# Kernel tuning notes

Measured on AMD Instinct MI355X. Metric: run time of the kernel, lower is better.

The kernel has to match this reference:

```python
import jax, jax.numpy as jnp
import numpy as np
from jax.scipy.ndimage import map_coordinates

# Geometry (parallel-beam analogue of the astra projector in the source)
NUMPIX = 256          # image is NUMPIX x NUMPIX
NUMBIN = 367          # detector bins (~ NUMPIX*sqrt(2), 1-pixel spacing)
NUMTHETA = 360        # projection angles over [0, 360) deg
NS = 4                # number of ordered subsets (angles j::NS per subset)
NT = 367              # samples along each ray (covers image diagonal)
BETA = 1.0            # relaxation parameter
DX = 1.0              # pixel size
THRESHOLD = 0.01      # IterativeLayer residual threshold
MAX_ITERS = 2         # IterativeLayer max_iterations
EPS = float(np.finfo(np.float64).eps)
DEN_EPS = 1e-6        # guard for Minv/Dinv denominators

_theta = np.deg2rad(np.arange(NUMTHETA) * (360.0 / NUMTHETA)).astype(np.float32)
_COS = jnp.asarray(np.cos(_theta), dtype=jnp.float32)
_SIN = jnp.asarray(np.sin(_theta), dtype=jnp.float32)
_CDET = (NUMBIN - 1) / 2.0
_CPIX = (NUMPIX - 1) / 2.0
_S = jnp.arange(NUMBIN, dtype=jnp.float32) - _CDET          # detector coords
_T = jnp.arange(NT, dtype=jnp.float32) - (NT - 1) / 2.0     # along-ray coords
_pix = jnp.arange(NUMPIX, dtype=jnp.float32) - _CPIX
_Y, _X = jnp.meshgrid(_pix, _pix, indexing='ij')            # pixel centers


def forward_project(f, ca, sa):
    # Radon transform of f for angles (ca, sa): line integral along each ray.
    # coords: [na, NUMBIN, NT]
    x = _S[None, :, None] * ca[:, None, None] - _T[None, None, :] * sa[:, None, None]
    y = _S[None, :, None] * sa[:, None, None] + _T[None, None, :] * ca[:, None, None]
    vals = map_coordinates(f, [y + _CPIX, x + _CPIX], order=1, mode='constant', cval=0.0)
    return vals.sum(-1)  # [na, NUMBIN]


def backproject(g, ca, sa):
    # Adjoint-style backprojection of sinogram g [na, NUMBIN] onto the image grid.
    def one(ga, c, s_):
        sd = _X * c + _Y * s_ + _CDET                      # [NUMPIX, NUMPIX]
        i0 = jnp.floor(sd)
        w = sd - i0
        i0i = i0.astype(jnp.int32)
        v0 = jnp.where((i0i >= 0) & (i0i < NUMBIN), ga[jnp.clip(i0i, 0, NUMBIN - 1)], 0.0)
        i1i = i0i + 1
        v1 = jnp.where((i1i >= 0) & (i1i < NUMBIN), ga[jnp.clip(i1i, 0, NUMBIN - 1)], 0.0)
        return v0 * (1.0 - w) + v1 * w
    return jax.vmap(one)(g, ca, sa).sum(0)


def sart_reconstruct(f, sino):
    # Precompute SART normalizers per subset: Minv = A_j(1_img), Dinv = A_j^T(1_sino).
    cas = [_COS[j::NS] for j in range(NS)]
    sas = [_SIN[j::NS] for j in range(NS)]
    ones_img = jnp.ones((NUMPIX, NUMPIX), dtype=f.dtype)
    Minv = [jnp.maximum(forward_project(ones_img, cas[j], sas[j]), DEN_EPS) for j in range(NS)]
    Dinv = [jnp.maximum(backproject(jnp.ones_like(sino[j::NS]), cas[j], sas[j]), DEN_EPS) for j in range(NS)]

    for _ in range(MAX_ITERS):
        # inner denoiser layer modeled as identity
        fk = f
        for j in range(NS):  # one SART ordered-subset sweep
            fp = forward_project(fk, cas[j], sas[j])
            diffs = (sino[j::NS] - fp * DX) / Minv[j] / DX
            bp = backproject(diffs, cas[j], sas[j])
            bp = jnp.where(jnp.abs(bp) > 1000.0, 0.0, bp)
            fk = fk + BETA * bp / Dinv[j]
        fk = jnp.maximum(fk, EPS)
        # residual ||A fk * dx - sino||_F, computed subset-by-subset
        res2 = jnp.float32(0.0)
        for j in range(NS):
            fpj = forward_project(fk, cas[j], sas[j])
            res2 = res2 + jnp.sum((fpj * DX - sino[j::NS]) ** 2)
        res = jnp.sqrt(res2)
        f = jnp.where(res > THRESHOLD, fk, f)
    return f


def setup_inputs() -> dict:
    key = jax.random.key(0)
    k1, k2 = jax.random.split(key)
    f0 = jax.random.uniform(k1, (NUMPIX, NUMPIX), dtype=jnp.float32)
    sino = jax.random.uniform(k2, (NUMTHETA, NUMBIN), dtype=jnp.float32)
    return {"f0": f0, "sino": sino}


def reference(f0, sino):
    return sart_reconstruct(f0, sino)
```

## Files before the change

kernel.cpp:

```cpp
#include <hip/hip_runtime.h>
#include <math.h>

#define NUMPIX 256
#define NUMBIN 367
#define NUMTHETA 360
#define NS 4
#define NT 367
#define NPIX2 (NUMPIX * NUMPIX)
#define NRAYS_ALL (NUMTHETA * NUMBIN)
#define NANG_SUB (NUMTHETA / NS)
#define NRAYS_SUB (NANG_SUB * NUMBIN)

#define NANG_HALF 180
#define NRAYS_HALF (NANG_HALF * NUMBIN)
#define NANG_SUBH (NANG_SUB / 2)
#define NRAYS_SUBH (NANG_SUBH * NUMBIN)

#define CDET 183.0f
#define CPIX 127.5f
#define TOFF 183.0f
#define DEN_EPS 1e-6f
#define EPS_F 2.2204460492503131e-16f
#define RES2_THRESH 1e-4f
#define INV_DINV (1.0f / 90.0f)

#define QW 260
#define QROWS 258
#define QN2 (QW * QROWS)
#define QNF (QN2 * 2)

#define HALF_BLOCKS ((NRAYS_HALF + 15) / 16)
#define SUBH_BLOCKS ((NRAYS_SUBH + 15) / 16)

typedef float f4q __attribute__((ext_vector_type(4), aligned(8)));
typedef float f2u __attribute__((ext_vector_type(2), aligned(4)));

#define OFF_COS   0
#define OFF_SIN   (OFF_COS + NUMTHETA)
#define OFF_MINV  (OFF_SIN + NUMTHETA)
#define OFF_RESP1 (OFF_MINV + NRAYS_ALL)
#define OFF_RESP2 (OFF_RESP1 + 4136)
#define OFF_Q     (OFF_RESP2 + 4136)
#define OFF_QT    (OFF_Q + QNF)
#define OFF_Q0    (OFF_QT + QNF)
#define OFF_QT0   (OFF_Q0 + QNF)
#define OFF_DIFF  (OFF_QT0 + QNF)
#define OFF_DIFFB (OFF_DIFF + NRAYS_SUB + 2)

__device__ __forceinline__ void clip_axis2(float c0, float rate,
                                           float bLo, float bHi,
                                           float& lo, float& hi) {
    if (fabsf(rate) > 1e-6f) {
        float inv = 1.0f / rate;
        float a = (bLo - c0) * inv;
        float b = (bHi - c0) * inv;
        lo = fmaxf(lo, fminf(a, b));
        hi = fminf(hi, fmaxf(a, b));
    } else if (c0 <= bLo || c0 >= bHi) {
        lo = 1e9f; hi = -1e9f;
    }
}

__device__ __forceinline__ int ray_chunks16(float x0, float y0, float ca, float sa,
                                            int& itlo) {
    float lo = -1e9f, hi = 1e9f;
    clip_axis2(x0, -sa, -2.0f, 257.0f, lo, hi);
    clip_axis2(y0,  ca, -2.0f, 257.0f, lo, hi);
    if (hi < lo) { itlo = 0; return 0; }
    int a = (int)floorf(lo + TOFF) - 1; if (a < 0) a = 0;
    int b = (int)ceilf(hi + TOFF) + 1;  if (b > NT - 1) b = NT - 1;
    itlo = a;
    if (b < a) return 0;
    return (b - a + 16) >> 4;
}

struct RaySetup {
    int angle, bin, ai, nc;
    float u, v, du, dv;
    bool useT;
};

__device__ __forceinline__ RaySetup ray_setup(int rr, int angleStart, int angleStride,
                                              const float* __restrict__ cosA,
                                              const float* __restrict__ sinA,
                                              int slane) {
    RaySetup R;
    R.ai = rr / NUMBIN;
    R.bin = rr - R.ai * NUMBIN;
    R.angle = angleStart + R.ai * angleStride;
    float ca = cosA[R.angle], sa = sinA[R.angle];
    float s = (float)R.bin - CDET;
    float x0 = fmaf(s, ca, CPIX);
    float y0 = fmaf(s, sa, CPIX);
    int itlo;
    R.nc = ray_chunks16(x0, y0, ca, sa, itlo);
    R.useT = fabsf(ca) > fabsf(sa);
    float u0 = R.useT ? y0 : x0, du = R.useT ? ca : -sa;
    float v0 = R.useT ? x0 : y0, dv = R.useT ? -sa : ca;
    float tt0 = (float)(itlo + slane) - TOFF;
    R.u = fmaf(tt0, du, u0);
    R.v = fmaf(tt0, dv, v0);
    R.du = du; R.dv = dv;
    return R;
}

template <bool DUAL>
__device__ __forceinline__ void march(const float* __restrict__ imgA,
                                      const float* __restrict__ imgB,
                                      float u, float v, float du, float dv,
                                      int nc, float& outA, float& outB) {
    const float du16 = du * 16.0f, dv16 = dv * 16.0f;
    const float du32 = du * 32.0f, dv32 = dv * 32.0f;
    float a0 = 0.0f, a1 = 0.0f, b0 = 0.0f, b1 = 0.0f;
    int ic = 0;
    for (; ic + 1 < nc; ic += 2) {
        float u1 = fminf(fmaxf(u, -1.0f), 256.0f);
        float v1 = fminf(fmaxf(v, -1.0f), 256.0f);
        float u2 = fminf(fmaxf(u + du16, -1.0f), 256.0f);
        float v2 = fminf(fmaxf(v + dv16, -1.0f), 256.0f);
        float fu1 = floorf(u1), fv1 = floorf(v1);
        float fu2 = floorf(u2), fv2 = floorf(v2);
        float wu1 = u1 - fu1, wv1 = v1 - fv1;
        float wu2 = u2 - fu2, wv2 = v2 - fv2;
        int idx1 = (int)fmaf(fv1, (float)QW, fu1);
        int idx2 = (int)fmaf(fv2, (float)QW, fu2);
        f4q qa1 = *(const f4q*)(imgA + idx1 * 2);
        f4q qa2 = *(const f4q*)(imgA + idx2 * 2);
        float t1 = fmaf(wu1, qa1.z - qa1.x, qa1.x);
        float c1 = fmaf(wu1, qa1.w - qa1.y, qa1.y);
        a0 += fmaf(wv1, c1 - t1, t1);
        float t2 = fmaf(wu2, qa2.z - qa2.x, qa2.x);
        float c2 = fmaf(wu2, qa2.w - qa2.y, qa2.y);
        a1 += fmaf(wv2, c2 - t2, t2);
        if (DUAL) {
            f4q qb1 = *(const f4q*)(imgB + idx1 * 2);
            f4q qb2 = *(const f4q*)(imgB + idx2 * 2);
            float s1 = fmaf(wu1, qb1.z - qb1.x, qb1.x);
            float d1 = fmaf(wu1, qb1.w - qb1.y, qb1.y);
            b0 += fmaf(wv1, d1 - s1, s1);
            float s2 = fmaf(wu2, qb2.z - qb2.x, qb2.x);
            float d2 = fmaf(wu2, qb2.w - qb2.y, qb2.y);
            b1 += fmaf(wv2, d2 - s2, s2);
        }
        u += du32; v += dv32;
    }
    if (ic < nc) {
        float u1 = fminf(fmaxf(u, -1.0f), 256.0f);
        float v1 = fminf(fmaxf(v, -1.0f), 256.0f);
        float fu1 = floorf(u1), fv1 = floorf(v1);
        float wu1 = u1 - fu1, wv1 = v1 - fv1;
        int idx1 = (int)fmaf(fv1, (float)QW, fu1);
        f4q qa1 = *(const f4q*)(imgA + idx1 * 2);
        float t1 = fmaf(wu1, qa1.z - qa1.x, qa1.x);
        float c1 = fmaf(wu1, qa1.w - qa1.y, qa1.y);
        a0 += fmaf(wv1, c1 - t1, t1);
        if (DUAL) {
            f4q qb1 = *(const f4q*)(imgB + idx1 * 2);
            float s1 = fmaf(wu1, qb1.z - qb1.x, qb1.x);
            float d1 = fmaf(wu1, qb1.w - qb1.y, qb1.y);
            b0 += fmaf(wv1, d1 - s1, s1);
        }
    }
    outA = a0 + a1;
    outB = b0 + b1;
}

__global__ __launch_bounds__(256)
void init_minv_kernel(float* __restrict__ cosA, float* __restrict__ sinA,
                      float* __restrict__ Qf, float* __restrict__ QTf,
                      float* __restrict__ Q0f, float* __restrict__ QT0f,
                      float* __restrict__ minv,
                      const float* __restrict__ f0) {
    int idx = blockIdx.x * blockDim.x + threadIdx.x;
    if (idx < NUMTHETA) {
        float th = (float)((double)idx * 0.017453292519943295);
        cosA[idx] = (float)cos((double)th);
        sinA[idx] = (float)sin((double)th);
    }
    if (idx < QN2) {
        int qr = idx / QW, qc = idx - qr * QW;
        int r = qr - 1, c = qc - 1;
        bool cv = ((unsigned)c < 256u);
        bool rv0 = ((unsigned)r < 256u), rv1 = ((unsigned)(r + 1) < 256u);
        float a = (cv && rv0) ? f0[r * NUMPIX + c] : 0.0f;
        float b = (cv && rv1) ? f0[(r + 1) * NUMPIX + c] : 0.0f;
        Qf[idx * 2] = a;  Qf[idx * 2 + 1] = b;
        Q0f[idx * 2] = a; Q0f[idx * 2 + 1] = b;
        float ta = (cv && rv0) ? f0[c * NUMPIX + r] : 0.0f;
        float tb = (cv && rv1) ? f0[c * NUMPIX + (r + 1)] : 0.0f;
        QTf[idx * 2] = ta;  QTf[idx * 2 + 1] = tb;
        QT0f[idx * 2] = ta; QT0f[idx * 2 + 1] = tb;
    }

    const int lane = threadIdx.x & 63;
    const int wid = threadIdx.x >> 6;
    const int sub = lane >> 4, slane = lane & 15;
    int ray = blockIdx.x * 16 + wid * 4 + sub;
    if (ray >= NRAYS_HALF) return;
    int angle = ray / NUMBIN;
    int bin = ray - angle * NUMBIN;
    float th = (float)((double)angle * 0.017453292519943295);
    float ca, sa;
    __sincosf(th, &sa, &ca);
    float s = (float)bin - CDET;
    float x0 = fmaf(s, ca, CPIX);
    float y0 = fmaf(s, sa, CPIX);
    float acc = 0.0f;
    int count = 0;
    float lo = -1e9f, hi = 1e9f;
    clip_axis2(x0, -sa, -2.0f, 257.0f, lo, hi);
    clip_axis2(y0,  ca, -2.0f, 257.0f, lo, hi);
    int e1a = 0, e1b = -1, e2a = 0, e2b = -1;
    if (hi >= lo) {
        int itA = (int)floorf(lo + TOFF) - 1; if (itA < 0) itA = 0;
        int itB = (int)ceilf(hi + TOFF) + 1;  if (itB > NT - 1) itB = NT - 1;
        if (itB >= itA) {
            float ilo = -1e9f, ihi = 1e9f;
            clip_axis2(x0, -sa, 0.05f, 254.95f, ilo, ihi);
            clip_axis2(y0,  ca, 0.05f, 254.95f, ilo, ihi);
            int jA = 1, jB = 0;
            if (ihi >= ilo) {
                jA = (int)ceilf(ilo + TOFF) + 1;
                jB = (int)floorf(ihi + TOFF) - 1;
                if (jA < itA) jA = itA;
                if (jB > itB) jB = itB;
            }
            if (jB >= jA) {
                count = jB - jA + 1;
                e1a = itA; e1b = jA - 1;
                e2a = jB + 1; e2b = itB;
            } else {
                e1a = itA; e1b = itB;
            }
        }
    }
    #pragma unroll 1
    for (int base = e1a; base <= e1b; base += 16) {
        int t = base + slane;
        float tt = (float)t - TOFF;
        float x = fmaf(-tt, sa, x0);
        float y = fmaf(tt, ca, y0);
        float fx = floorf(x), fy = floorf(y);
        float wx = x - fx, wy = y - fy;
        int c0 = (int)fx, r0 = (int)fy;
        float ux = (((unsigned)c0 < 256u) ? (1.0f - wx) : 0.0f) +
                   (((unsigned)(c0 + 1) < 256u) ? wx : 0.0f);
        float uy = (((unsigned)r0 < 256u) ? (1.0f - wy) : 0.0f) +
                   (((unsigned)(r0 + 1) < 256u) ? wy : 0.0f);
        if (t <= e1b) acc += ux * uy;
    }
    #pragma unroll 1
    for (int base = e2a; base <= e2b; base += 16) {
        int t = base + slane;
        float tt = (float)t - TOFF;
        float x = fmaf(-tt, sa, x0);
        float y = fmaf(tt, ca, y0);
        float fx = floorf(x), fy = floorf(y);
        float wx = x - fx, wy = y - fy;
        int c0 = (int)fx, r0 = (int)fy;
        float ux = (((unsigned)c0 < 256u) ? (1.0f - wx) : 0.0f) +
                   (((unsigned)(c0 + 1) < 256u) ? wx : 0.0f);
        float uy = (((unsigned)r0 < 256u) ? (1.0f - wy) : 0.0f) +
                   (((unsigned)(r0 + 1) < 256u) ? wy : 0.0f);
        if (t <= e2b) acc += ux * uy;
    }
    acc += __shfl_down(acc, 8, 16);
    acc += __shfl_down(acc, 4, 16);
    acc += __shfl_down(acc, 2, 16);
    acc += __shfl_down(acc, 1, 16);
    if (slane == 0) {
        float m = fmaxf(acc + (float)count, DEN_EPS);
        minv[angle * NUMBIN + bin] = m;
        minv[(angle + NANG_HALF) * NUMBIN + (NUMBIN - 1 - bin)] = m;
    }
}

__device__ __forceinline__ float res_block_partial(
        int unit, const float* __restrict__ Qn, const float* __restrict__ Qt,
        const float* __restrict__ sino,
        const float* __restrict__ cosA, const float* __restrict__ sinA,
        float* partLds) {
    const int wid = threadIdx.x >> 6, lane = threadIdx.x & 63;
    const int sub = lane >> 4, slane = lane & 15;
    int ray = unit * 16 + wid * 4 + sub;
    bool valid = ray < NRAYS_HALF;
    int rr = valid ? ray : NRAYS_HALF - 1;
    RaySetup R = ray_setup(rr, 0, 1, cosA, sinA, slane);
    const float* img = (R.useT ? Qt : Qn) + (QW + 1) * 2;
    float acc, dum;
    march<false>(img, img, R.u, R.v, R.du, R.dv, valid ? R.nc : 0, acc, dum);
    acc += __shfl_down(acc, 8, 16);
    acc += __shfl_down(acc, 4, 16);
    acc += __shfl_down(acc, 2, 16);
    acc += __shfl_down(acc, 1, 16);
    float d2 = 0.0f;
    if (slane == 0 && valid) {
        float d = acc - sino[R.angle * NUMBIN + R.bin];
        int a2 = R.angle + NANG_HALF;
        int b2 = NUMBIN - 1 - R.bin;
        float dm = acc - sino[a2 * NUMBIN + b2];
        d2 = d * d + dm * dm;
    }
    d2 += __shfl_down(d2, 16);
    d2 += __shfl_down(d2, 32);
    if (lane == 0) partLds[wid] = d2;
    __syncthreads();
    return partLds[0] + partLds[1] + partLds[2] + partLds[3];
}

__global__ __launch_bounds__(256)
void fp_sub_kernel(const float* __restrict__ Qn, const float* __restrict__ Qt,
                   const float* __restrict__ sino, const float* __restrict__ minv,
                   float* __restrict__ gOut,
                   const float* __restrict__ cosA, const float* __restrict__ sinA,
                   int j) {
    const int wid = threadIdx.x >> 6, lane = threadIdx.x & 63;
    const int sub = lane >> 4, slane = lane & 15;
    int ray = blockIdx.x * 16 + wid * 4 + sub;
    bool valid = ray < NRAYS_SUBH;
    int rr = valid ? ray : NRAYS_SUBH - 1;
    RaySetup R = ray_setup(rr, j, NS, cosA, sinA, slane);
    const float* img = (R.useT ? Qt : Qn) + (QW + 1) * 2;
    float acc, dum;
    march<false>(img, img, R.u, R.v, R.du, R.dv, valid ? R.nc : 0, acc, dum);
    acc += __shfl_down(acc, 8, 16);
    acc += __shfl_down(acc, 4, 16);
    acc += __shfl_down(acc, 2, 16);
    acc += __shfl_down(acc, 1, 16);
    if (slane == 0 && valid) {
        gOut[R.ai * NUMBIN + R.bin] =
            (sino[R.angle * NUMBIN + R.bin] - acc) /
            minv[R.angle * NUMBIN + R.bin];
        int a2 = R.angle + NANG_HALF;
        int b2 = NUMBIN - 1 - R.bin;
        gOut[(R.ai + NANG_SUBH) * NUMBIN + b2] =
            (sino[a2 * NUMBIN + b2] - acc) /
            minv[a2 * NUMBIN + b2];
    }
}

__global__ __launch_bounds__(256)
void fp_merged_kernel(const float* __restrict__ Qn, const float* __restrict__ Qt,
                      const float* __restrict__ Q0n, const float* __restrict__ Q0t,
                      const float* __restrict__ sino, const float* __restrict__ minv,
                      float* __restrict__ gA, float* __restrict__ gB,
                      const float* __restrict__ cosA, const float* __restrict__ sinA,
                      float* __restrict__ resP1) {
    __shared__ float part[4];
    int bid = blockIdx.x;
    if (bid < HALF_BLOCKS) {
        float tot = res_block_partial(bid, Qn, Qt, sino, cosA, sinA, part);
        if (threadIdx.x == 0) resP1[bid] = tot;
        return;
    }
    int bid2 = bid - HALF_BLOCKS;
    const int wid = threadIdx.x >> 6, lane = threadIdx.x & 63;
    const int sub = lane >> 4, slane = lane & 15;
    int ray = bid2 * 16 + wid * 4 + sub;
    bool valid = ray < NRAYS_SUBH;
    int rr = valid ? ray : NRAYS_SUBH - 1;
    RaySetup R = ray_setup(rr, 0, NS, cosA, sinA, slane);
    const float* imgA = (R.useT ? Qt : Qn) + (QW + 1) * 2;
    const float* imgB = (R.useT ? Q0t : Q0n) + (QW + 1) * 2;
    float accA, accB;
    march<true>(imgA, imgB, R.u, R.v, R.du, R.dv, valid ? R.nc : 0, accA, accB);
    accA += __shfl_down(accA, 8, 16);
    accB += __shfl_down(accB, 8, 16);
    accA += __shfl_down(accA, 4, 16);
    accB += __shfl_down(accB, 4, 16);
    accA += __shfl_down(accA, 2, 16);
    accB += __shfl_down(accB, 2, 16);
    accA += __shfl_down(accA, 1, 16);
    accB += __shfl_down(accB, 1, 16);
    if (slane == 0 && valid) {
        float m1 = minv[R.angle * NUMBIN + R.bin];
        float s1 = sino[R.angle * NUMBIN + R.bin];
        gA[R.ai * NUMBIN + R.bin] = (s1 - accA) / m1;
        gB[R.ai * NUMBIN + R.bin] = (s1 - accB) / m1;
        int a2 = R.angle + NANG_HALF;
        int b2 = NUMBIN - 1 - R.bin;
        float m2 = minv[a2 * NUMBIN + b2];
        float s2 = sino[a2 * NUMBIN + b2];
        gA[(R.ai + NANG_SUBH) * NUMBIN + b2] = (s2 - accA) / m2;
        gB[(R.ai + NANG_SUBH) * NUMBIN + b2] = (s2 - accB) / m2;
    }
}

__global__ __launch_bounds__(256)
void fp_res2_kernel(const float* __restrict__ Qn, const float* __restrict__ Qt,
                    const float* __restrict__ sino,
                    const float* __restrict__ cosA, const float* __restrict__ sinA,
                    float* __restrict__ resP2) {
    __shared__ float part[4];
    float tot = res_block_partial(blockIdx.x, Qn, Qt, sino, cosA, sinA, part);
    if (threadIdx.x == 0) resP2[blockIdx.x] = tot;
}

__global__ __launch_bounds__(256)
void select_kernel(float* __restrict__ fcur,
                   const float* __restrict__ Qn, const float* __restrict__ f0,
                   const float* __restrict__ resP1,
                   const float* __restrict__ resP2) {
    __shared__ float b1[4], b2[4];
    const int tid = threadIdx.x;
    float a1 = 0.0f, a2 = 0.0f;
    for (int i = tid; i < HALF_BLOCKS; i += 256) {
        a1 += resP1[i];
        a2 += resP2[i];
    }
    #pragma unroll
    for (int off = 32; off; off >>= 1) {
        a1 += __shfl_down(a1, off);
        a2 += __shfl_down(a2, off);
    }
    if ((tid & 63) == 0) { b1[tid >> 6] = a1; b2[tid >> 6] = a2; }
    __syncthreads();
    bool upd1 = (b1[0] + b1[1] + b1[2] + b1[3]) > RES2_THRESH;
    bool upd2 = (b2[0] + b2[1] + b2[2] + b2[3]) > RES2_THRESH;
    int p = blockIdx.x * 256 + tid;
    int px = p & (NUMPIX - 1), py = p >> 8;
    float v = upd2 ? Qn[((py + 1) * QW + (px + 1)) * 2]
                   : (upd1 ? fcur[p] : f0[p]);
    fcur[p] = v;
}

__global__ __launch_bounds__(256)
void bp_update_kernel(float* __restrict__ Qf, float* __restrict__ QTf,
                      const float* __restrict__ Q0f,
                      const float* __restrict__ gA, const float* __restrict__ gB,
                      const float* __restrict__ cosA, const float* __restrict__ sinA,
                      const float* __restrict__ resP1, float* __restrict__ fcur,
                      int j, int doClamp, int writeFcur, int chooseFlag) {
    __shared__ float part[4][64];
    const float* g = gA;
    const float* src = Qf;
    if (chooseFlag) {
        __shared__ float rbuf[4];
        float a = 0.0f;
        for (int i = threadIdx.x; i < HALF_BLOCKS; i += 256) a += resP1[i];
        #pragma unroll
        for (int off = 32; off; off >>= 1) a += __shfl_down(a, off);
        if ((threadIdx.x & 63) == 0) rbuf[threadIdx.x >> 6] = a;
        __syncthreads();
        float r1v = rbuf[0] + rbuf[1] + rbuf[2] + rbuf[3];
        if (!(r1v > RES2_THRESH)) { g = gB; src = Q0f; }
    }
    const int tx = threadIdx.x & 63;
    const int ty = threadIdx.x >> 6;
    int p = blockIdx.x * 64 + tx;
    int px = p & (NUMPIX - 1), py = p >> 8;
    float X = (float)px - CPIX, Y = (float)py - CPIX;
    float acc = 0.0f;
    for (int i = ty; i < NANG_SUBH; i += 4) {
        int angle = j + NS * i;
        float ca = cosA[angle], sa = sinA[angle];
        float sd = fmaf(X, ca, fmaf(Y, sa, CDET));
        float fl = floorf(sd);
        float w = sd - fl;
        int i0 = (int)fl;
        f2u gv = *(const f2u*)(g + i * NUMBIN + i0);
        acc += fmaf(w, gv.y - gv.x, gv.x);
        f2u gw = *(const f2u*)(g + (i + NANG_SUBH) * NUMBIN + (365 - i0));
        acc += fmaf(w, gw.x - gw.y, gw.y);
    }
    part[ty][tx] = acc;
    __syncthreads();
    if (ty == 0) {
        float s = part[0][tx] + part[1][tx] + part[2][tx] + part[3][tx];
        float bp = (fabsf(s) > 1000.0f) ? 0.0f : s;
        float v = src[((py + 1) * QW + (px + 1)) * 2] + bp * INV_DINV;
        if (doClamp) v = fmaxf(v, EPS_F);
        Qf[((py + 1) * QW + (px + 1)) * 2]      = v;
        Qf[(py * QW + (px + 1)) * 2 + 1]        = v;
        QTf[((px + 1) * QW + (py + 1)) * 2]     = v;
        QTf[(px * QW + (py + 1)) * 2 + 1]       = v;
        if (writeFcur) fcur[p] = v;
    }
}

extern "C" void kernel_launch(void* const* d_in, const int* in_sizes, int n_in,
                              void* d_out, int out_size, void* d_ws, size_t ws_size,
                              hipStream_t stream) {
    const float* f0 = (const float*)d_in[0];
    const float* sino = (const float*)d_in[1];
    float* fcur = (float*)d_out;
    float* ws = (float*)d_ws;

    float* cosA = ws + OFF_COS;
    float* sinA = ws + OFF_SIN;
    float* minv = ws + OFF_MINV;
    float* resP1 = ws + OFF_RESP1;
    float* resP2 = ws + OFF_RESP2;
    float* Qf   = ws + OFF_Q;
    float* QTf  = ws + OFF_QT;
    float* Q0f  = ws + OFF_Q0;
    float* QT0f = ws + OFF_QT0;
    float* dfA  = ws + OFF_DIFF;
    float* dfB  = ws + OFF_DIFFB;

    init_minv_kernel<<<HALF_BLOCKS, 256, 0, stream>>>(
        cosA, sinA, Qf, QTf, Q0f, QT0f, minv, f0);

    for (int j = 0; j < NS; j++) {
        fp_sub_kernel<<<SUBH_BLOCKS, 256, 0, stream>>>(
            Qf, QTf, sino, minv, dfA, cosA, sinA, j);
        bp_update_kernel<<<NPIX2 / 64, 256, 0, stream>>>(
            Qf, QTf, Q0f, dfA, dfB, cosA, sinA, resP1, fcur,
            j, (j == NS - 1) ? 1 : 0, (j == NS - 1) ? 1 : 0, 0);
    }
    fp_merged_kernel<<<HALF_BLOCKS + SUBH_BLOCKS, 256, 0, stream>>>(
        Qf, QTf, Q0f, QT0f, sino, minv, dfA, dfB, cosA, sinA, resP1);
    bp_update_kernel<<<NPIX2 / 64, 256, 0, stream>>>(
        Qf, QTf, Q0f, dfA, dfB, cosA, sinA, resP1, fcur,
        0, 0, 0, 1);
    for (int j = 1; j < NS; j++) {
        fp_sub_kernel<<<SUBH_BLOCKS, 256, 0, stream>>>(
            Qf, QTf, sino, minv, dfA, cosA, sinA, j);
        bp_update_kernel<<<NPIX2 / 64, 256, 0, stream>>>(
            Qf, QTf, Q0f, dfA, dfB, cosA, sinA, resP1, fcur,
            j, (j == NS - 1) ? 1 : 0, 0, 0);
    }
    fp_res2_kernel<<<HALF_BLOCKS, 256, 0, stream>>>(
        Qf, QTf, sino, cosA, sinA, resP2);
    select_kernel<<<NPIX2 / 256, 256, 0, stream>>>(
        fcur, Qf, f0, resP1, resP2);
}
```

Baseline: 232.8 us.

## Fuse first forward projection into init, merge residual and select via last-block atomics

The first subset's forward projection of f0 is computed inside the Minv init kernel, which removes one fp_sub launch. The Q0/QT0 image copies and the dual march are dropped; the fallback path reads f0 directly. The final residual kernel and select kernel are merged with per-slot atomics and a last-block completion counter, and rays are re-indexed per angle with 23 units of 16 bins. These changes cut launches and memory traffic, at the cost of atomic counters and a more complex control flow.

New measurement: 254.2 us. 9.2% more time.

```diff
diff --git a/kernel.cpp b/kernel.cpp
--- a/kernel.cpp
+++ b/kernel.cpp
@@ -7,14 +7,15 @@
 #define NS 4
 #define NT 367
 #define NPIX2 (NUMPIX * NUMPIX)
-#define NRAYS_ALL (NUMTHETA * NUMBIN)
 #define NANG_SUB (NUMTHETA / NS)
 #define NRAYS_SUB (NANG_SUB * NUMBIN)
 
 #define NANG_HALF 180
-#define NRAYS_HALF (NANG_HALF * NUMBIN)
 #define NANG_SUBH (NANG_SUB / 2)
-#define NRAYS_SUBH (NANG_SUBH * NUMBIN)
+
+#define UPA 23
+#define HALF_UNITS (NANG_HALF * UPA)
+#define SUB_UNITS  (NANG_SUBH * UPA)
 
 #define CDET 183.0f
 #define CPIX 127.5f
@@ -29,23 +30,20 @@
 #define QN2 (QW * QROWS)
 #define QNF (QN2 * 2)
 
-#define HALF_BLOCKS ((NRAYS_HALF + 15) / 16)
-#define SUBH_BLOCKS ((NRAYS_SUBH + 15) / 16)
-
 typedef float f4q __attribute__((ext_vector_type(4), aligned(8)));
 typedef float f2u __attribute__((ext_vector_type(2), aligned(4)));
 
-#define OFF_COS   0
-#define OFF_SIN   (OFF_COS + NUMTHETA)
-#define OFF_MINV  (OFF_SIN + NUMTHETA)
-#define OFF_RESP1 (OFF_MINV + NRAYS_ALL)
-#define OFF_RESP2 (OFF_RESP1 + 4136)
-#define OFF_Q     (OFF_RESP2 + 4136)
-#define OFF_QT    (OFF_Q + QNF)
-#define OFF_Q0    (OFF_QT + QNF)
-#define OFF_QT0   (OFF_Q0 + QNF)
-#define OFF_DIFF  (OFF_QT0 + QNF)
-#define OFF_DIFFB (OFF_DIFF + NRAYS_SUB + 2)
+#define OFF_COS    0
+#define OFF_SIN    (OFF_COS + NUMTHETA)
+#define OFF_MINV   (OFF_SIN + NUMTHETA)
+#define OFF_RESP1  (OFF_MINV + NUMTHETA * NUMBIN)
+#define OFF_RESACC (OFF_RESP1 + HALF_UNITS + 4)
+#define OFF_CNT    (OFF_RESACC + 2048)
+#define OFF_FIN    (OFF_CNT + 2048)
+#define OFF_Q      (OFF_FIN + 8)
+#define OFF_QT     (OFF_Q + QNF)
+#define OFF_DIFF   (OFF_QT + QNF)
+#define OFF_DIFF0  (OFF_DIFF + NRAYS_SUB + 2)
 
 __device__ __forceinline__ void clip_axis2(float c0, float rate,
                                            float bLo, float bHi,
@@ -75,21 +73,18 @@
 }
 
 struct RaySetup {
-    int angle, bin, ai, nc;
+    int nc;
     float u, v, du, dv;
     bool useT;
 };
 
-__device__ __forceinline__ RaySetup ray_setup(int rr, int angleStart, int angleStride,
-                                              const float* __restrict__ cosA,
-                                              const float* __restrict__ sinA,
-                                              int slane) {
+__device__ __forceinline__ RaySetup ray_setup_ab(int angle, int bin,
+                                                 const float* __restrict__ cosA,
+                                                 const float* __restrict__ sinA,
+                                                 int slane) {
     RaySetup R;
-    R.ai = rr / NUMBIN;
-    R.bin = rr - R.ai * NUMBIN;
-    R.angle = angleStart + R.ai * angleStride;
-    float ca = cosA[R.angle], sa = sinA[R.angle];
-    float s = (float)R.bin - CDET;
+    float ca = cosA[angle], sa = sinA[angle];
+    float s = (float)bin - CDET;
     float x0 = fmaf(s, ca, CPIX);
     float y0 = fmaf(s, sa, CPIX);
     int itlo;
@@ -104,14 +99,12 @@
     return R;
 }
 
-template <bool DUAL>
-__device__ __forceinline__ void march(const float* __restrict__ imgA,
-                                      const float* __restrict__ imgB,
-                                      float u, float v, float du, float dv,
-                                      int nc, float& outA, float& outB) {
+__device__ __forceinline__ float march(const float* __restrict__ img,
+                                       float u, float v, float du, float dv,
+                                       int nc) {
     const float du16 = du * 16.0f, dv16 = dv * 16.0f;
     const float du32 = du * 32.0f, dv32 = dv * 32.0f;
-    float a0 = 0.0f, a1 = 0.0f, b0 = 0.0f, b1 = 0.0f;
+    float a0 = 0.0f, a1 = 0.0f;
     int ic = 0;
     for (; ic + 1 < nc; ic += 2) {
         float u1 = fminf(fmaxf(u, -1.0f), 256.0f);
@@ -124,24 +117,14 @@
         float wu2 = u2 - fu2, wv2 = v2 - fv2;
         int idx1 = (int)fmaf(fv1, (float)QW, fu1);
         int idx2 = (int)fmaf(fv2, (float)QW, fu2);
-        f4q qa1 = *(const f4q*)(imgA + idx1 * 2);
-        f4q qa2 = *(const f4q*)(imgA + idx2 * 2);
+        f4q qa1 = *(const f4q*)(img + idx1 * 2);
+        f4q qa2 = *(const f4q*)(img + idx2 * 2);
         float t1 = fmaf(wu1, qa1.z - qa1.x, qa1.x);
         float c1 = fmaf(wu1, qa1.w - qa1.y, qa1.y);
         a0 += fmaf(wv1, c1 - t1, t1);
         float t2 = fmaf(wu2, qa2.z - qa2.x, qa2.x);
         float c2 = fmaf(wu2, qa2.w - qa2.y, qa2.y);
         a1 += fmaf(wv2, c2 - t2, t2);
-        if (DUAL) {
-            f4q qb1 = *(const f4q*)(imgB + idx1 * 2);
-            f4q qb2 = *(const f4q*)(imgB + idx2 * 2);
-            float s1 = fmaf(wu1, qb1.z - qb1.x, qb1.x);
-            float d1 = fmaf(wu1, qb1.w - qb1.y, qb1.y);
-            b0 += fmaf(wv1, d1 - s1, s1);
-            float s2 = fmaf(wu2, qb2.z - qb2.x, qb2.x);
-            float d2 = fmaf(wu2, qb2.w - qb2.y, qb2.y);
-            b1 += fmaf(wv2, d2 - s2, s2);
-        }
         u += du32; v += dv32;
     }
     if (ic < nc) {
@@ -150,27 +133,59 @@
         float fu1 = floorf(u1), fv1 = floorf(v1);
         float wu1 = u1 - fu1, wv1 = v1 - fv1;
         int idx1 = (int)fmaf(fv1, (float)QW, fu1);
-        f4q qa1 = *(const f4q*)(imgA + idx1 * 2);
+        f4q qa1 = *(const f4q*)(img + idx1 * 2);
         float t1 = fmaf(wu1, qa1.z - qa1.x, qa1.x);
         float c1 = fmaf(wu1, qa1.w - qa1.y, qa1.y);
         a0 += fmaf(wv1, c1 - t1, t1);
-        if (DUAL) {
-            f4q qb1 = *(const f4q*)(imgB + idx1 * 2);
-            float s1 = fmaf(wu1, qb1.z - qb1.x, qb1.x);
-            float d1 = fmaf(wu1, qb1.w - qb1.y, qb1.y);
-            b0 += fmaf(wv1, d1 - s1, s1);
-        }
-    }
-    outA = a0 + a1;
-    outB = b0 + b1;
+    }
+    return a0 + a1;
+}
+
+__device__ __forceinline__ float res_block_total(
+        int unit, const float* __restrict__ Qn, const float* __restrict__ Qt,
+        const float* __restrict__ sino,
+        const float* __restrict__ cosA, const float* __restrict__ sinA,
+        float* partLds, const float* __restrict__ minv, float* __restrict__ gA) {
+    const int wid = threadIdx.x >> 6, lane = threadIdx.x & 63;
+    const int sub = lane >> 4, slane = lane & 15;
+    int angle = unit / UPA;
+    int bin = (unit - angle * UPA) * 16 + wid * 4 + sub;
+    bool valid = bin < NUMBIN;
+    RaySetup R = ray_setup_ab(angle, valid ? bin : 0, cosA, sinA, slane);
+    const float* img = (R.useT ? Qt : Qn) + (QW + 1) * 2;
+    float acc = march(img, R.u, R.v, R.du, R.dv, valid ? R.nc : 0);
+    acc += __shfl_down(acc, 8, 16);
+    acc += __shfl_down(acc, 4, 16);
+    acc += __shfl_down(acc, 2, 16);
+    acc += __shfl_down(acc, 1, 16);
+    float d2 = 0.0f;
+    if (slane == 0 && valid) {
+        int b2 = NUMBIN - 1 - bin;
+        float s1 = sino[angle * NUMBIN + bin];
+        float s2 = sino[(angle + NANG_HALF) * NUMBIN + b2];
+        float d = acc - s1, dm = acc - s2;
+        d2 = d * d + dm * dm;
+        if (gA != nullptr && (angle & 3) == 0) {
+            int ai = angle >> 2;
+            gA[ai * NUMBIN + bin] = (s1 - acc) / minv[angle * NUMBIN + bin];
+            gA[(ai + NANG_SUBH) * NUMBIN + b2] =
+                (s2 - acc) / minv[(angle + NANG_HALF) * NUMBIN + b2];
+        }
+    }
+    d2 += __shfl_down(d2, 16);
+    d2 += __shfl_down(d2, 32);
+    if (lane == 0) partLds[wid] = d2;
+    __syncthreads();
+    return partLds[0] + partLds[1] + partLds[2] + partLds[3];
 }
 
 __global__ __launch_bounds__(256)
 void init_minv_kernel(float* __restrict__ cosA, float* __restrict__ sinA,
                       float* __restrict__ Qf, float* __restrict__ QTf,
-                      float* __restrict__ Q0f, float* __restrict__ QT0f,
                       float* __restrict__ minv,
-                      const float* __restrict__ f0) {
+                      float* __restrict__ dfA, float* __restrict__ df0,
+                      const float* __restrict__ f0,
+                      const float* __restrict__ sino) {
     int idx = blockIdx.x * blockDim.x + threadIdx.x;
     if (idx < NUMTHETA) {
         float th = (float)((double)idx * 0.017453292519943295);
@@ -185,20 +200,82 @@
         float a = (cv && rv0) ? f0[r * NUMPIX + c] : 0.0f;
         float b = (cv && rv1) ? f0[(r + 1) * NUMPIX + c] : 0.0f;
         Qf[idx * 2] = a;  Qf[idx * 2 + 1] = b;
-        Q0f[idx * 2] = a; Q0f[idx * 2 + 1] = b;
         float ta = (cv && rv0) ? f0[c * NUMPIX + r] : 0.0f;
         float tb = (cv && rv1) ? f0[c * NUMPIX + (r + 1)] : 0.0f;
         QTf[idx * 2] = ta;  QTf[idx * 2 + 1] = tb;
-        QT0f[idx * 2] = ta; QT0f[idx * 2 + 1] = tb;
     }
 
     const int lane = threadIdx.x & 63;
     const int wid = threadIdx.x >> 6;
     const int sub = lane >> 4, slane = lane & 15;
-    int ray = blockIdx.x * 16 + wid * 4 + sub;
-    if (ray >= NRAYS_HALF) return;
-    int angle = ray / NUMBIN;
-    int bin = ray - angle * NUMBIN;
+    int unit = blockIdx.x;
+    int angle = unit / UPA;
+    int bin = (unit - angle * UPA) * 16 + wid * 4 + sub;
+    bool valid = bin < NUMBIN;
+
+    if ((angle & 3) == 0) {
+        double thd = (double)angle * 0.017453292519943295;
+        float ca = (float)cos(thd);
+        float sa = (float)sin(thd);
+        float s = (float)bin - CDET;
+        float x0 = fmaf(s, ca, CPIX);
+        float y0 = fmaf(s, sa, CPIX);
+        float lo = -1e9f, hi = 1e9f;
+        clip_axis2(x0, -sa, -2.0f, 257.0f, lo, hi);
+        clip_axis2(y0,  ca, -2.0f, 257.0f, lo, hi);
+        float val = 0.0f, wsum = 0.0f;
+        if (hi >= lo) {
+            int itA = (int)floorf(lo + TOFF) - 1; if (itA < 0) itA = 0;
+            int itB = (int)ceilf(hi + TOFF) + 1;  if (itB > NT - 1) itB = NT - 1;
+            #pragma unroll 1
+            for (int base = itA; base <= itB; base += 16) {
+                int t = base + slane;
+                float tt = (float)t - TOFF;
+                float x = fmaf(-tt, sa, x0);
+                float y = fmaf(tt, ca, y0);
+                float fx = floorf(x), fy = floorf(y);
+                float wx = x - fx, wy = y - fy;
+                int c0 = (int)fx, r0 = (int)fy;
+                float ux0 = ((unsigned)c0 < 256u) ? (1.0f - wx) : 0.0f;
+                float ux1 = ((unsigned)(c0 + 1) < 256u) ? wx : 0.0f;
+                float uy0 = ((unsigned)r0 < 256u) ? (1.0f - wy) : 0.0f;
+                float uy1 = ((unsigned)(r0 + 1) < 256u) ? wy : 0.0f;
+                int c0c = c0 < 0 ? 0 : (c0 > 255 ? 255 : c0);
+                int c1c = c0 + 1 < 0 ? 0 : (c0 + 1 > 255 ? 255 : c0 + 1);
+                int r0c = r0 < 0 ? 0 : (r0 > 255 ? 255 : r0);
+                int r1c = r0 + 1 < 0 ? 0 : (r0 + 1 > 255 ? 255 : r0 + 1);
+                float F00 = f0[r0c * NUMPIX + c0c];
+                float F01 = f0[r0c * NUMPIX + c1c];
+                float F10 = f0[r1c * NUMPIX + c0c];
+                float F11 = f0[r1c * NUMPIX + c1c];
+                if (t <= itB) {
+                    val += uy0 * fmaf(ux0, F00, ux1 * F01)
+                         + uy1 * fmaf(ux0, F10, ux1 * F11);
+                    wsum += (ux0 + ux1) * (uy0 + uy1);
+                }
+            }
+        }
+        #pragma unroll
+        for (int off = 8; off; off >>= 1) {
+            val  += __shfl_down(val, off, 16);
+            wsum += __shfl_down(wsum, off, 16);
+        }
+        if (slane == 0 && valid) {
+            float m = fmaxf(wsum, DEN_EPS);
+            int b2 = NUMBIN - 1 - bin;
+            minv[angle * NUMBIN + bin] = m;
+            minv[(angle + NANG_HALF) * NUMBIN + b2] = m;
+            int ai = angle >> 2;
+            float g1 = (sino[angle * NUMBIN + bin] - val) / m;
+            float g2 = (sino[(angle + NANG_HALF) * NUMBIN + b2] - val) / m;
+            dfA[ai * NUMBIN + bin] = g1;
+            df0[ai * NUMBIN + bin] = g1;
+            dfA[(ai + NANG_SUBH) * NUMBIN + b2] = g2;
+            df0[(ai + NANG_SUBH) * NUMBIN + b2] = g2;
+        }
+        return;
+    }
+
     float th = (float)((double)angle * 0.017453292519943295);
     float ca, sa;
     __sincosf(th, &sa, &ca);
@@ -268,44 +345,11 @@
     acc += __shfl_down(acc, 4, 16);
     acc += __shfl_down(acc, 2, 16);
     acc += __shfl_down(acc, 1, 16);
-    if (slane == 0) {
+    if (slane == 0 && valid) {
         float m = fmaxf(acc + (float)count, DEN_EPS);
         minv[angle * NUMBIN + bin] = m;
         minv[(angle + NANG_HALF) * NUMBIN + (NUMBIN - 1 - bin)] = m;
     }
-}
-
-__device__ __forceinline__ float res_block_partial(
-        int unit, const float* __restrict__ Qn, const float* __restrict__ Qt,
-        const float* __restrict__ sino,
-        const float* __restrict__ cosA, const float* __restrict__ sinA,
-        float* partLds) {
-    const int wid = threadIdx.x >> 6, lane = threadIdx.x & 63;
-    const int sub = lane >> 4, slane = lane & 15;
-    int ray = unit * 16 + wid * 4 + sub;
-    bool valid = ray < NRAYS_HALF;
-    int rr = valid ? ray : NRAYS_HALF - 1;
-    RaySetup R = ray_setup(rr, 0, 1, cosA, sinA, slane);
-    const float* img = (R.useT ? Qt : Qn) + (QW + 1) * 2;
-    float acc, dum;
-    march<false>(img, img, R.u, R.v, R.du, R.dv, valid ? R.nc : 0, acc, dum);
-    acc += __shfl_down(acc, 8, 16);
-    acc += __shfl_down(acc, 4, 16);
-    acc += __shfl_down(acc, 2, 16);
-    acc += __shfl_down(acc, 1, 16);
-    float d2 = 0.0f;
-    if (slane == 0 && valid) {
-        float d = acc - sino[R.angle * NUMBIN + R.bin];
-        int a2 = R.angle + NANG_HALF;
-        int b2 = NUMBIN - 1 - R.bin;
-        float dm = acc - sino[a2 * NUMBIN + b2];
-        d2 = d * d + dm * dm;
-    }
-    d2 += __shfl_down(d2, 16);
-    d2 += __shfl_down(d2, 32);
-    if (lane == 0) partLds[wid] = d2;
-    __syncthreads();
-    return partLds[0] + partLds[1] + partLds[2] + partLds[3];
 }
 
 __global__ __launch_bounds__(256)
@@ -316,140 +360,142 @@
                    int j) {
     const int wid = threadIdx.x >> 6, lane = threadIdx.x & 63;
     const int sub = lane >> 4, slane = lane & 15;
-    int ray = blockIdx.x * 16 + wid * 4 + sub;
-    bool valid = ray < NRAYS_SUBH;
-    int rr = valid ? ray : NRAYS_SUBH - 1;
-    RaySetup R = ray_setup(rr, j, NS, cosA, sinA, slane);
+    int unit = blockIdx.x;
+    int ai = unit / UPA;
+    int bin = (unit - ai * UPA) * 16 + wid * 4 + sub;
+    bool valid = bin < NUMBIN;
+    int angle = j + NS * ai;
+    RaySetup R = ray_setup_ab(angle, valid ? bin : 0, cosA, sinA, slane);
     const float* img = (R.useT ? Qt : Qn) + (QW + 1) * 2;
-    float acc, dum;
-    march<false>(img, img, R.u, R.v, R.du, R.dv, valid ? R.nc : 0, acc, dum);
+    float acc = march(img, R.u, R.v, R.du, R.dv, valid ? R.nc : 0);
     acc += __shfl_down(acc, 8, 16);
     acc += __shfl_down(acc, 4, 16);
     acc += __shfl_down(acc, 2, 16);
     acc += __shfl_down(acc, 1, 16);
     if (slane == 0 && valid) {
-        gOut[R.ai * NUMBIN + R.bin] =
-            (sino[R.angle * NUMBIN + R.bin] - acc) /
-            minv[R.angle * NUMBIN + R.bin];
-        int a2 = R.angle + NANG_HALF;
-        int b2 = NUMBIN - 1 - R.bin;
-        gOut[(R.ai + NANG_SUBH) * NUMBIN + b2] =
-            (sino[a2 * NUMBIN + b2] - acc) /
-            minv[a2 * NUMBIN + b2];
+        int b2 = NUMBIN - 1 - bin;
+        int a2 = angle + NANG_HALF;
+        gOut[ai * NUMBIN + bin] =
+            (sino[angle * NUMBIN + bin] - acc) / minv[angle * NUMBIN + bin];
+        gOut[(ai + NANG_SUBH) * NUMBIN + b2] =
+            (sino[a2 * NUMBIN + b2] - acc) / minv[a2 * NUMBIN + b2];
     }
 }
 
 __global__ __launch_bounds__(256)
 void fp_merged_kernel(const float* __restrict__ Qn, const float* __restrict__ Qt,
-                      const float* __restrict__ Q0n, const float* __restrict__ Q0t,
                       const float* __restrict__ sino, const float* __restrict__ minv,
-                      float* __restrict__ gA, float* __restrict__ gB,
+                      float* __restrict__ gA,
                       const float* __restrict__ cosA, const float* __restrict__ sinA,
                       float* __restrict__ resP1) {
     __shared__ float part[4];
-    int bid = blockIdx.x;
-    if (bid < HALF_BLOCKS) {
-        float tot = res_block_partial(bid, Qn, Qt, sino, cosA, sinA, part);
-        if (threadIdx.x == 0) resP1[bid] = tot;
-        return;
-    }
-    int bid2 = bid - HALF_BLOCKS;
-    const int wid = threadIdx.x >> 6, lane = threadIdx.x & 63;
-    const int sub = lane >> 4, slane = lane & 15;
-    int ray = bid2 * 16 + wid * 4 + sub;
-    bool valid = ray < NRAYS_SUBH;
-    int rr = valid ? ray : NRAYS_SUBH - 1;
-    RaySetup R = ray_setup(rr, 0, NS, cosA, sinA, slane);
-    const float* imgA = (R.useT ? Qt : Qn) + (QW + 1) * 2;
-    const float* imgB = (R.useT ? Q0t : Q0n) + (QW + 1) * 2;
-    float accA, accB;
-    march<true>(imgA, imgB, R.u, R.v, R.du, R.dv, valid ? R.nc : 0, accA, accB);
-    accA += __shfl_down(accA, 8, 16);
-    accB += __shfl_down(accB, 8, 16);
-    accA += __shfl_down(accA, 4, 16);
-    accB += __shfl_down(accB, 4, 16);
-    accA += __shfl_down(accA, 2, 16);
-    accB += __shfl_down(accB, 2, 16);
-    accA += __shfl_down(accA, 1, 16);
-    accB += __shfl_down(accB, 1, 16);
-    if (slane == 0 && valid) {
-        float m1 = minv[R.angle * NUMBIN + R.bin];
-        float s1 = sino[R.angle * NUMBIN + R.bin];
-        gA[R.ai * NUMBIN + R.bin] = (s1 - accA) / m1;
-        gB[R.ai * NUMBIN + R.bin] = (s1 - accB) / m1;
-        int a2 = R.angle + NANG_HALF;
-        int b2 = NUMBIN - 1 - R.bin;
-        float m2 = minv[a2 * NUMBIN + b2];
-        float s2 = sino[a2 * NUMBIN + b2];
-        gA[(R.ai + NANG_SUBH) * NUMBIN + b2] = (s2 - accA) / m2;
-        gB[(R.ai + NANG_SUBH) * NUMBIN + b2] = (s2 - accB) / m2;
-    }
+    float tot = res_block_total(blockIdx.x, Qn, Qt, sino, cosA, sinA, part,
+                                minv, gA);
+    if (threadIdx.x == 0) resP1[blockIdx.x] = tot;
 }
 
 __global__ __launch_bounds__(256)
-void fp_res2_kernel(const float* __restrict__ Qn, const float* __restrict__ Qt,
-                    const float* __restrict__ sino,
-                    const float* __restrict__ cosA, const float* __restrict__ sinA,
-                    float* __restrict__ resP2) {
+void fp_res2_sel_kernel(const float* __restrict__ Qn, const float* __restrict__ Qt,
+                        const float* __restrict__ sino,
+                        const float* __restrict__ cosA, const float* __restrict__ sinA,
+                        const float* __restrict__ resP1,
+                        float* __restrict__ resAcc, unsigned* __restrict__ cntp,
+                        unsigned* __restrict__ finp,
+                        float* __restrict__ fcur, const float* __restrict__ f0) {
     __shared__ float part[4];
-    float tot = res_block_partial(blockIdx.x, Qn, Qt, sino, cosA, sinA, part);
-    if (threadIdx.x == 0) resP2[blockIdx.x] = tot;
-}
-
-__global__ __launch_bounds__(256)
-void select_kernel(float* __restrict__ fcur,
-                   const float* __restrict__ Qn, const float* __restrict__ f0,
-                   const float* __restrict__ resP1,
-                   const float* __restrict__ resP2) {
-    __shared__ float b1[4], b2[4];
-    const int tid = threadIdx.x;
-    float a1 = 0.0f, a2 = 0.0f;
-    for (int i = tid; i < HALF_BLOCKS; i += 256) {
-        a1 += resP1[i];
-        a2 += resP2[i];
-    }
-    #pragma unroll
-    for (int off = 32; off; off >>= 1) {
-        a1 += __shfl_down(a1, off);
-        a2 += __shfl_down(a2, off);
-    }
-    if ((tid & 63) == 0) { b1[tid >> 6] = a1; b2[tid >> 6] = a2; }
+    __shared__ int lastFlag;
+    __shared__ float sres[2];
+    float tot = res_block_total(blockIdx.x, Qn, Qt, sino, cosA, sinA, part,
+                                nullptr, nullptr);
+    if (threadIdx.x == 0) {
+        int slot = blockIdx.x & 63;
+        atomicAdd(&resAcc[slot * 32], tot);
+        asm volatile("s_waitcnt vmcnt(0)" ::: "memory");
+        unsigned slotCnt = (HALF_UNITS >> 6) +
+                           ((slot < (HALF_UNITS & 63)) ? 1u : 0u);
+        unsigned old = atomicAdd(&cntp[slot * 32], 1u);
+        int last = 0;
+        if (old == slotCnt - 1u) {
+            asm volatile("s_waitcnt vmcnt(0)" ::: "memory");
+            unsigned o2 = atomicAdd(finp, 1u);
+            last = (o2 == 63u);
+        }
+        lastFlag = last;
+    }
     __syncthreads();
-    bool upd1 = (b1[0] + b1[1] + b1[2] + b1[3]) > RES2_THRESH;
-    bool upd2 = (b2[0] + b2[1] + b2[2] + b2[3]) > RES2_THRESH;
-    int p = blockIdx.x * 256 + tid;
-    int px = p & (NUMPIX - 1), py = p >> 8;
-    float v = upd2 ? Qn[((py + 1) * QW + (px + 1)) * 2]
-                   : (upd1 ? fcur[p] : f0[p]);
-    fcur[p] = v;
+    if (!lastFlag) return;
+
+    {
+        float v = 0.0f;
+        if (threadIdx.x < 64) v = atomicAdd(&resAcc[threadIdx.x * 32], 0.0f);
+        #pragma unroll
+        for (int off = 32; off; off >>= 1) v += __shfl_down(v, off);
+        if (threadIdx.x == 0) sres[1] = v;
+    }
+    {
+        __shared__ float b1[4];
+        float a = 0.0f;
+        for (int i = threadIdx.x; i < HALF_UNITS; i += 256) a += resP1[i];
+        #pragma unroll
+        for (int off = 32; off; off >>= 1) a += __shfl_down(a, off);
+        if ((threadIdx.x & 63) == 0) b1[threadIdx.x >> 6] = a;
+        __syncthreads();
+        if (threadIdx.x == 0) sres[0] = b1[0] + b1[1] + b1[2] + b1[3];
+    }
+    __syncthreads();
+    bool upd1 = sres[0] > RES2_THRESH;
+    bool upd2 = sres[1] > RES2_THRESH;
+    int py = threadIdx.x;
+    float* frow = fcur + py * NUMPIX;
+    if (upd2) {
+        const float* qbase = Qn + ((py + 1) * QW + 1) * 2;
+        for (int px = 0; px < NUMPIX; px += 2) {
+            f4q q = *(const f4q*)(qbase + px * 2);
+            f2u w; w.x = q.x; w.y = q.z;
+            *(f2u*)(frow + px) = w;
+        }
+    } else if (!upd1) {
+        const float* f0row = f0 + py * NUMPIX;
+        for (int px = 0; px < NUMPIX; px += 2)
+            *(f2u*)(frow + px) = *(const f2u*)(f0row + px);
+    }
 }
 
 __global__ __launch_bounds__(256)
 void bp_update_kernel(float* __restrict__ Qf, float* __restrict__ QTf,
-                      const float* __restrict__ Q0f,
+                      const float* __restrict__ f0,
                       const float* __restrict__ gA, const float* __restrict__ gB,
                       const float* __restrict__ cosA, const float* __restrict__ sinA,
                       const float* __restrict__ resP1, float* __restrict__ fcur,
-                      int j, int doClamp, int writeFcur, int chooseFlag) {
+                      float* __restrict__ resAcc, unsigned* __restrict__ cntp,
+                      unsigned* __restrict__ finp,
+                      int j, int doClamp, int writeFcur, int chooseFlag,
+                      int zeroFin) {
     __shared__ float part[4][64];
+    if (zeroFin && blockIdx.x == 0) {
+        int t = threadIdx.x;
+        if (t < 64) { resAcc[t * 32] = 0.0f; cntp[t * 32] = 0u; }
+        if (t == 64) *finp = 0u;
+    }
     const float* g = gA;
-    const float* src = Qf;
+    bool hot = true;
     if (chooseFlag) {
         __shared__ float rbuf[4];
         float a = 0.0f;
-        for (int i = threadIdx.x; i < HALF_BLOCKS; i += 256) a += resP1[i];
+        for (int i = threadIdx.x; i < HALF_UNITS; i += 256) a += resP1[i];
         #pragma unroll
         for (int off = 32; off; off >>= 1) a += __shfl_down(a, off);
         if ((threadIdx.x & 63) == 0) rbuf[threadIdx.x >> 6] = a;
         __syncthreads();
         float r1v = rbuf[0] + rbuf[1] + rbuf[2] + rbuf[3];
-        if (!(r1v > RES2_THRESH)) { g = gB; src = Q0f; }
+        if (!(r1v > RES2_THRESH)) { g = gB; hot = false; }
     }
     const int tx = threadIdx.x & 63;
     const int ty = threadIdx.x >> 6;
     int p = blockIdx.x * 64 + tx;
     int px = p & (NUMPIX - 1), py = p >> 8;
     float X = (float)px - CPIX, Y = (float)py - CPIX;
+    float base = hot ? Qf[((py + 1) * QW + (px + 1)) * 2] : f0[p];
     float acc = 0.0f;
     for (int i = ty; i < NANG_SUBH; i += 4) {
         int angle = j + NS * i;
@@ -465,15 +511,17 @@
     }
     part[ty][tx] = acc;
     __syncthreads();
+    float s = part[0][tx] + part[1][tx] + part[2][tx] + part[3][tx];
+    float bpv = (fabsf(s) > 1000.0f) ? 0.0f : s;
+    float v = base + bpv * INV_DINV;
+    if (doClamp) v = fmaxf(v, EPS_F);
     if (ty == 0) {
-        float s = part[0][tx] + part[1][tx] + part[2][tx] + part[3][tx];
-        float bp = (fabsf(s) > 1000.0f) ? 0.0f : s;
-        float v = src[((py + 1) * QW + (px + 1)) * 2] + bp * INV_DINV;
-        if (doClamp) v = fmaxf(v, EPS_F);
-        Qf[((py + 1) * QW + (px + 1)) * 2]      = v;
-        Qf[(py * QW + (px + 1)) * 2 + 1]        = v;
-        QTf[((px + 1) * QW + (py + 1)) * 2]     = v;
-        QTf[(px * QW + (py + 1)) * 2 + 1]       = v;
+        Qf[((py + 1) * QW + (px + 1)) * 2]  = v;
+        Qf[(py * QW + (px + 1)) * 2 + 1]    = v;
+    } else if (ty == 1) {
+        QTf[((px + 1) * QW + (py + 1)) * 2] = v;
+        QTf[(px * QW + (py + 1)) * 2 + 1]   = v;
+    } else if (ty == 2) {
         if (writeFcur) fcur[p] = v;
     }
 }
@@ -490,38 +538,41 @@
     float* sinA = ws + OFF_SIN;
     float* minv = ws + OFF_MINV;
     float* resP1 = ws + OFF_RESP1;
-    float* resP2 = ws + OFF_RESP2;
+    float* resAcc = ws + OFF_RESACC;
+    unsigned* cntp = (unsigned*)(ws + OFF_CNT);
+    unsigned* finp = (unsigned*)(ws + OFF_FIN);
     float* Qf   = ws + OFF_Q;
     float* QTf  = ws + OFF_QT;
-    float* Q0f  = ws + OFF_Q0;
-    float* QT0f = ws + OFF_QT0;
     float* dfA  = ws + OFF_DIFF;
-    float* dfB  = ws + OFF_DIFFB;
-
-    init_minv_kernel<<<HALF_BLOCKS, 256, 0, stream>>>(
-        cosA, sinA, Qf, QTf, Q0f, QT0f, minv, f0);
-
-    for (int j = 0; j < NS; j++) {
-        fp_sub_kernel<<<SUBH_BLOCKS, 256, 0, stream>>>(
+    float* df0  = ws + OFF_DIFF0;
+
+    init_minv_kernel<<<HALF_UNITS, 256, 0, stream>>>(
+        cosA, sinA, Qf, QTf, minv, dfA, df0, f0, sino);
+
+    bp_update_kernel<<<NPIX2 / 64, 256, 0, stream>>>(
+        Qf, QTf, f0, dfA, df0, cosA, sinA, resP1, fcur,
+        resAcc, cntp, finp, 0, 0, 0, 0, 0);
+    for (int j = 1; j < NS; j++) {
+        fp_sub_kernel<<<SUB_UNITS, 256, 0, stream>>>(
             Qf, QTf, sino, minv, dfA, cosA, sinA, j);
         bp_update_kernel<<<NPIX2 / 64, 256, 0, stream>>>(
-            Qf, QTf, Q0f, dfA, dfB, cosA, sinA, resP1, fcur,
-            j, (j == NS - 1) ? 1 : 0, (j == NS - 1) ? 1 : 0, 0);
-    }
-    fp_merged_kernel<<<HALF_BLOCKS + SUBH_BLOCKS, 256, 0, stream>>>(
-        Qf, QTf, Q0f, QT0f, sino, minv, dfA, dfB, cosA, sinA, resP1);
+            Qf, QTf, f0, dfA, df0, cosA, sinA, resP1, fcur,
+            resAcc, cntp, finp,
+            j, (j == NS - 1) ? 1 : 0, (j == NS - 1) ? 1 : 0, 0, 0);
+    }
+    fp_merged_kernel<<<HALF_UNITS, 256, 0, stream>>>(
+        Qf, QTf, sino, minv, dfA, cosA, sinA, resP1);
     bp_update_kernel<<<NPIX2 / 64, 256, 0, stream>>>(
-        Qf, QTf, Q0f, dfA, dfB, cosA, sinA, resP1, fcur,
-        0, 0, 0, 1);
+        Qf, QTf, f0, dfA, df0, cosA, sinA, resP1, fcur,
+        resAcc, cntp, finp, 0, 0, 0, 1, 0);
     for (int j = 1; j < NS; j++) {
-        fp_sub_kernel<<<SUBH_BLOCKS, 256, 0, stream>>>(
+        fp_sub_kernel<<<SUB_UNITS, 256, 0, stream>>>(
             Qf, QTf, sino, minv, dfA, cosA, sinA, j);
         bp_update_kernel<<<NPIX2 / 64, 256, 0, stream>>>(
-            Qf, QTf, Q0f, dfA, dfB, cosA, sinA, resP1, fcur,
-            j, (j == NS - 1) ? 1 : 0, 0, 0);
-    }
-    fp_res2_kernel<<<HALF_BLOCKS, 256, 0, stream>>>(
-        Qf, QTf, sino, cosA, sinA, resP2);
-    select_kernel<<<NPIX2 / 256, 256, 0, stream>>>(
-        fcur, Qf, f0, resP1, resP2);
-}
+            Qf, QTf, f0, dfA, df0, cosA, sinA, resP1, fcur,
+            resAcc, cntp, finp,
+            j, (j == NS - 1) ? 1 : 0, 0, 0, (j == NS - 1) ? 1 : 0);
+    }
+    fp_res2_sel_kernel<<<HALF_UNITS, 256, 0, stream>>>(
+        Qf, QTf, sino, cosA, sinA, resP1, resAcc, cntp, finp, fcur, f0);
+}
```
